# Kernel tuning notes

Measured on AMD Instinct MI355X. Metric: run time of the kernel, lower is better.

## Reference

```python
import jax, jax.numpy as jnp
import numpy as np

B, LAT, H, O, T = 512, 128, 1024, 1, 256


def setup_inputs() -> dict:
    key = jax.random.key(0)
    ks = jax.random.split(key, 8)

    def p(k, shape, fan_in):
        return (jax.random.normal(k, shape, dtype=jnp.float32) / np.sqrt(fan_in)).astype(jnp.float32)

    return {
        "z": jax.random.normal(ks[0], (B, LAT), dtype=jnp.float32),
        # fc_z_to_h / fc_z_to_c
        "Wzh": p(ks[1], (H, LAT), LAT), "bzh": jnp.zeros((H,), jnp.float32),
        "Wzc": p(ks[2], (H, LAT), LAT), "bzc": jnp.zeros((H,), jnp.float32),
        # LSTM (single layer), PyTorch gate order i,f,g,o stacked along dim 0
        "W_ih": p(ks[3], (4 * H, O), max(O, 1)),
        "W_hh": p(ks[4], (4 * H, H), H),
        "b_ih": jnp.zeros((4 * H,), jnp.float32),
        "b_hh": jnp.zeros((4 * H,), jnp.float32),
        # fc_out
        "W_out": p(ks[5], (O, H), H), "b_out": jnp.zeros((O,), jnp.float32),
        "tgt_len": T,
    }


def reference(z, Wzh, bzh, Wzc, bzc, W_ih, W_hh, b_ih, b_hh, W_out, b_out, tgt_len):
    # initial states from latent code
    h = jnp.tanh(z @ Wzh.T + bzh)            # (B, H)
    c = jnp.tanh(z @ Wzc.T + bzc)            # (B, H)
    x0 = jnp.zeros((z.shape[0], W_ih.shape[1]), z.dtype)  # (B, O) zeros start token
    b = b_ih + b_hh

    def step(carry, _):
        h, c, x = carry
        gates = x @ W_ih.T + h @ W_hh.T + b  # (B, 4H)
        i, f, g, o = jnp.split(gates, 4, axis=-1)
        i = jax.nn.sigmoid(i)
        f = jax.nn.sigmoid(f)
        g = jnp.tanh(g)
        o = jax.nn.sigmoid(o)
        c_new = f * c + i * g
        h_new = o * jnp.tanh(c_new)
        y = h_new @ W_out.T + b_out
        return (h_new, c_new, y), y

    _, ys = jax.lax.scan(step, (h, c, x0), None, length=tgt_len)  # (T, B, O)
    return jnp.transpose(ys, (1, 0, 2))      # (B, T, O)
```

## Files before the change

### kernel.cpp

```cpp
#include <hip/hip_runtime.h>

typedef unsigned short u16;
typedef unsigned int u32;
typedef __bf16 bf16x8 __attribute__((ext_vector_type(8)));
typedef float f32x4 __attribute__((ext_vector_type(4)));
typedef u16 u16x8 __attribute__((ext_vector_type(8)));

#define AS1 __attribute__((address_space(1)))
#define AS3 __attribute__((address_space(3)))

constexpr int Bsz = 512;
constexpr int LATn = 128;
constexpr int Hn  = 1024;
constexpr int G4H = 4096;
constexpr int NBLK = 256;

__device__ __forceinline__ u16 f2bf(float x){
  u32 u = __float_as_uint(x);
  return (u16)((u + 0x7FFFu + ((u >> 16) & 1u)) >> 16);
}
__device__ __forceinline__ float bf2f(u16 h){ return __uint_as_float(((u32)h) << 16); }

__device__ __forceinline__ float sigm(float x){
  float e = __builtin_amdgcn_exp2f(x * -1.44269504088896f);
  return __builtin_amdgcn_rcpf(1.0f + e);
}
__device__ __forceinline__ float tanh_f(float x){
  float e = __builtin_amdgcn_exp2f(x * -2.88539008177793f);
  return __builtin_amdgcn_rcpf(1.0f + e) * 2.0f - 1.0f;
}

__device__ __forceinline__ bf16x8 ld8(const u16* p){
  u16x8 v = *reinterpret_cast<const u16x8*>(p);
  return __builtin_bit_cast(bf16x8, v);
}
__device__ __forceinline__ bf16x8 vld8(const volatile u16* p){
  u16x8 v = *reinterpret_cast<const volatile u16x8*>(p);
  return __builtin_bit_cast(bf16x8, v);
}

__device__ __forceinline__ void load16_lds(const u16* g, u16* l){
  __builtin_amdgcn_global_load_lds((AS1 void*)(u16*)g, (AS3 void*)l, 16, 0, 0);
}

__global__ void repack_kernel(
    const float* __restrict__ Whh, const float* __restrict__ b_ih, const float* __restrict__ b_hh,
    const float* __restrict__ Wih, const float* __restrict__ Wout, const float* __restrict__ bout,
    u16* wp, float* bpack, float* wihpack)
{
  const int idx0 = blockIdx.x * blockDim.x + threadIdx.x;
  const int stride = gridDim.x * blockDim.x;
  const float bo = bout[0];
  for (int i = idx0; i < G4H * Hn; i += stride){
    int row = i >> 10, k = i & 1023;
    int g = row >> 10, jj = row & 1023;
    int drow = (jj >> 4) * 64 + g * 16 + (jj & 15);
    float x = Whh[i] + Wout[k] * Wih[row];
    wp[drow * 1024 + k] = f2bf(x);
  }
  for (int i = idx0; i < G4H; i += stride){
    int g = i >> 10, jj = i & 1023;
    int drow = (jj >> 4) * 64 + g * 16 + (jj & 15);
    bpack[drow] = b_ih[i] + b_hh[i] + bo * Wih[i];
    wihpack[drow] = Wih[i];
  }
}

__global__ __launch_bounds__(256, 1) void init_kernel(
    const float* __restrict__ z,
    const float* __restrict__ Wzh, const float* __restrict__ bzh,
    const float* __restrict__ Wzc, const float* __restrict__ bzc,
    const float* __restrict__ Wout, const float* __restrict__ bout,
    u16* hb_hi, u16* hb_lo, float* cbuf, float* yinit)
{
  __shared__ float zrow[LATn];
  __shared__ float yred[256];
  const int b = blockIdx.x, tid = threadIdx.x;
  if (tid < LATn) zrow[tid] = z[b * LATn + tid];
  __syncthreads();
  float ysum = 0.f;
  #pragma unroll
  for (int jj = 0; jj < 4; ++jj){
    const int j = tid * 4 + jj;
    const float* wh = Wzh + (size_t)j * LATn;
    const float* wc = Wzc + (size_t)j * LATn;
    float sh = bzh[j], sc = bzc[j];
    for (int k = 0; k < LATn; ++k){
      const float zv = zrow[k];
      sh = fmaf(zv, wh[k], sh);
      sc = fmaf(zv, wc[k], sc);
    }
    const float h0 = tanh_f(sh);
    cbuf[(size_t)b * Hn + j] = tanh_f(sc);
    const u16 hi = f2bf(h0);
    hb_hi[(size_t)b * Hn + j] = hi;
    hb_lo[(size_t)b * Hn + j] = f2bf(h0 - bf2f(hi));
    ysum = fmaf(h0, Wout[j], ysum);
  }
  yred[tid] = ysum;
  __syncthreads();
  for (int s = 128; s > 0; s >>= 1){
    if (tid < s) yred[tid] += yred[tid + s];
    __syncthreads();
  }
  if (tid == 0) yinit[b] = yred[0] + bout[0];
}

__global__ __launch_bounds__(512, 1) void lstm_xcd(
    const u16* __restrict__ wp,
    const float* __restrict__ bpack, const float* __restrict__ wihpack,
    const float* __restrict__ Wout, const float* __restrict__ bout,
    const float* __restrict__ yinit,
    u16* __restrict__ hb_hi, u16* __restrict__ hb_lo,
    const float* __restrict__ cbuf, float* __restrict__ ypart,
    float* __restrict__ outp, const int* __restrict__ tlen,
    u32* claim, volatile u32* flags)
{
  __shared__ __align__(16) u16 ldsB[4][16384];
  __shared__ int sh_ids[2];

  const int tid = threadIdx.x;
  const int lane = tid & 63, w = tid >> 6;
  const int r = lane & 15, q = lane >> 4;
  const int rowg = w >> 1, jt = w & 1;
  const int T = tlen[0];

  if (tid == 0){
    const int xcd_ = (int)(__builtin_amdgcn_s_getreg(6164) & 7);
    const int slot_ = (int)atomicAdd(&claim[xcd_ * 16], 1u);
    sh_ids[0] = xcd_; sh_ids[1] = slot_;
  }
  __syncthreads();
  const int xcd = sh_ids[0];
  const int slot = sh_ids[1] & 31;

  const int jcol0 = slot * 128;
  const int j = slot * 32 + jt * 16 + r;
  const int row0x = xcd * 64;
  const int wrow0 = row0x + rowg * 16;

  volatile u32* myflag = flags + (size_t)(xcd * 32 + slot) * 16;
  volatile u32* gflag  = flags + (size_t)(xcd * 32) * 16;

  float bias_r[4], wih_r[4];
  #pragma unroll
  for (int nt = 0; nt < 4; ++nt){
    bias_r[nt] = bpack[jcol0 + jt * 64 + nt * 16 + r];
    wih_r[nt]  = wihpack[jcol0 + jt * 64 + nt * 16 + r];
  }
  const float wout_r = Wout[j];
  const float bo = bout[0];

  float creg[4];
  #pragma unroll
  for (int e = 0; e < 4; ++e)
    creg[e] = cbuf[(size_t)(wrow0 + q * 4 + e) * Hn + j];

  const u16* wph = wp + (size_t)jcol0 * 1024;

  auto stage = [&](int c){
    const int buf = c & 3;
    #pragma unroll
    for (int i = 0; i < 4; ++i){
      const int idx = i * 512 + tid;
      const int col = idx >> 4, sp = idx & 15;
      const int sgk = (sp ^ (col & 7)) * 8;
      const int dst = (i * 512 + w * 64) * 8;
      load16_lds(wph + (size_t)col * 1024 + c * 128 + sgk, &ldsB[buf][dst]);
    }
  };

  stage(0); stage(1); stage(2);

  #pragma unroll 1
  for (int t = 0; t < T; ++t){
    const int pb = t & 1;
    const u16* hs_hi = hb_hi + pb * (Bsz * Hn);
    const u16* hs_lo = hb_lo + pb * (Bsz * Hn);
    u16* hd_hi = hb_hi + (pb ^ 1) * (Bsz * Hn);
    u16* hd_lo = hb_lo + (pb ^ 1) * (Bsz * Hn);

    f32x4 acc[4];
    #pragma unroll
    for (int nt = 0; nt < 4; ++nt)
      #pragma unroll
      for (int e = 0; e < 4; ++e)
        acc[nt][e] = bias_r[nt];
    if (t == 0){
      #pragma unroll
      for (int e = 0; e < 4; ++e){
        const float yi = yinit[wrow0 + q * 4 + e];
        #pragma unroll
        for (int nt = 0; nt < 4; ++nt)
          acc[nt][e] -= yi * wih_r[nt];
      }
    }

    const volatile u16* ha_hi = hs_hi + (size_t)(wrow0 + r) * Hn + q * 8;
    const volatile u16* ha_lo = hs_lo + (size_t)(wrow0 + r) * Hn + q * 8;

    #pragma unroll
    for (int c = 0; c < 8; ++c){
      if (c == 0)      asm volatile("s_waitcnt vmcnt(8)"  ::: "memory");
      else if (c == 1) asm volatile("s_waitcnt vmcnt(16)" ::: "memory");
      else if (c == 2) asm volatile("s_waitcnt vmcnt(24)" ::: "memory");
      else if (c <= 5) asm volatile("s_waitcnt vmcnt(32)" ::: "memory");
      else if (c == 6) asm volatile("s_waitcnt vmcnt(28)" ::: "memory");
      else             asm volatile("s_waitcnt vmcnt(24)" ::: "memory");
      __builtin_amdgcn_s_barrier();
      asm volatile("" ::: "memory");

      if (c < 5) stage(c + 3);

      const int buf = c & 3;
      #pragma unroll
      for (int kc = 0; kc < 4; ++kc){
        const int ko = c * 128 + kc * 32;
        const bf16x8 ah = vld8(ha_hi + ko);
        const bf16x8 al = vld8(ha_lo + ko);
        #pragma unroll
        for (int nt = 0; nt < 4; ++nt){
          const int cc = jt * 64 + nt * 16 + r;
          const int phys = (kc * 4 + q) ^ (cc & 7);
          const bf16x8 bh = ld8(&ldsB[buf][(cc * 16 + phys) * 8]);
          acc[nt] = __builtin_amdgcn_mfma_f32_16x16x32_bf16(ah, bh, acc[nt], 0, 0, 0);
          acc[nt] = __builtin_amdgcn_mfma_f32_16x16x32_bf16(al, bh, acc[nt], 0, 0, 0);
        }
      }
    }

    float pp[4];
    #pragma unroll
    for (int e = 0; e < 4; ++e){
      const float gi = sigm(acc[0][e]);
      const float gf = sigm(acc[1][e]);
      const float gg = tanh_f(acc[2][e]);
      const float go = sigm(acc[3][e]);
      const float cn = gf * creg[e] + gi * gg;
      creg[e] = cn;
      const float hn = go * tanh_f(cn);
      const int row = wrow0 + q * 4 + e;
      const u16 hi = f2bf(hn);
      hd_hi[(size_t)row * Hn + j] = hi;
      hd_lo[(size_t)row * Hn + j] = f2bf(hn - bf2f(hi));
      pp[e] = hn * wout_r;
    }
    #pragma unroll
    for (int m = 1; m < 16; m <<= 1)
      #pragma unroll
      for (int e = 0; e < 4; ++e)
        pp[e] += __shfl_xor(pp[e], m, 64);
    if (r == 0){
      #pragma unroll
      for (int e = 0; e < 4; ++e){
        const int row_l = rowg * 16 + q * 4 + e;
        ypart[((size_t)(pb * 8 + xcd) * 64 + row_l) * 64 + slot * 2 + jt] = pp[e];
      }
    }

    __syncthreads();
    if (tid == 0) *myflag = (u32)(t + 1);
    if (t < T - 1){ stage(0); stage(1); stage(2); }

    if (w == 0){
      const u32 tgt = (u32)(t + 1);
      for (int spin = 0; spin < (1 << 17); ++spin){
        const u32 f = (lane < 32) ? gflag[(size_t)lane * 16] : tgt;
        if (__all(f >= tgt)) break;
        __builtin_amdgcn_s_sleep(1);
      }
    }
    __syncthreads();

    if (tid < 64){
      const int rsel = lane >> 5, ll = lane & 31;
      const int row_l = slot * 2 + rsel;
      const volatile float* yp = ypart + ((size_t)(pb * 8 + xcd) * 64 + row_l) * 64;
      float v = yp[ll] + yp[ll + 32];
      #pragma unroll
      for (int m = 1; m < 32; m <<= 1) v += __shfl_xor(v, m, 64);
      if (ll == 0) outp[(size_t)(row0x + row_l) * T + t] = v + bo;
    }
  }
}

extern "C" void kernel_launch(void* const* d_in, const int* in_sizes, int n_in,
                              void* d_out, int out_size, void* d_ws, size_t ws_size,
                              hipStream_t stream)
{
  const float* z    = (const float*)d_in[0];
  const float* Wzh  = (const float*)d_in[1];
  const float* bzh  = (const float*)d_in[2];
  const float* Wzc  = (const float*)d_in[3];
  const float* bzc  = (const float*)d_in[4];
  const float* Wih  = (const float*)d_in[5];
  const float* Whh  = (const float*)d_in[6];
  const float* b_ih = (const float*)d_in[7];
  const float* b_hh = (const float*)d_in[8];
  const float* Wout = (const float*)d_in[9];
  const float* bout = (const float*)d_in[10];
  const int*   tlen = (const int*)d_in[11];
  float* outp = (float*)d_out;

  char* ws = (char*)d_ws;
  size_t off = 0;
  auto alloc = [&](size_t bytes) -> char* {
    char* p = ws + off;
    off += (bytes + 255) & ~size_t(255);
    return p;
  };
  u16* wp     = (u16*)alloc((size_t)G4H * Hn * 2);
  u16* hb_hi  = (u16*)alloc((size_t)2 * Bsz * Hn * 2);
  u16* hb_lo  = (u16*)alloc((size_t)2 * Bsz * Hn * 2);
  float* cbuf    = (float*)alloc((size_t)Bsz * Hn * 4);
  float* yinit   = (float*)alloc((size_t)Bsz * 4);
  float* bpack   = (float*)alloc((size_t)G4H * 4);
  float* wihpack = (float*)alloc((size_t)G4H * 4);
  float* ypart   = (float*)alloc((size_t)2 * 8 * 64 * 64 * 4);
  u32* claim     = (u32*)alloc(8 * 16 * 4);
  u32* flags     = (u32*)alloc((size_t)8 * 32 * 16 * 4);

  (void)hipMemsetAsync(claim, 0, 8 * 16 * 4, stream);
  (void)hipMemsetAsync(flags, 0, (size_t)8 * 32 * 16 * 4, stream);

  repack_kernel<<<dim3(1024), dim3(256), 0, stream>>>(
      Whh, b_ih, b_hh, Wih, Wout, bout, wp, bpack, wihpack);

  init_kernel<<<dim3(Bsz), dim3(256), 0, stream>>>(
      z, Wzh, bzh, Wzc, bzc, Wout, bout, hb_hi, hb_lo, cbuf, yinit);

  lstm_xcd<<<dim3(NBLK), dim3(512), 0, stream>>>(
      wp, bpack, wihpack, Wout, bout, yinit,
      hb_hi, hb_lo, cbuf, ypart, outp, tlen, claim, flags);
}
```

Baseline: 6.860 ms.

## Prefetch h fragments three chunks ahead and split LDS weight tiles by k-half

```diff
diff --git a/kernel.cpp b/kernel.cpp
--- a/kernel.cpp
+++ b/kernel.cpp
@@ -116,7 +116,7 @@
     float* __restrict__ outp, const int* __restrict__ tlen,
     u32* claim, volatile u32* flags)
 {
-  __shared__ __align__(16) u16 ldsB[4][16384];
+  __shared__ __align__(16) u16 ldsB[4][2][8192];
   __shared__ int sh_ids[2];
 
   const int tid = threadIdx.x;
@@ -160,13 +160,15 @@
 
   auto stage = [&](int c){
     const int buf = c & 3;
+    u16* base = (u16*)ldsB[buf];
     #pragma unroll
     for (int i = 0; i < 4; ++i){
-      const int idx = i * 512 + tid;
-      const int col = idx >> 4, sp = idx & 15;
-      const int sgk = (sp ^ (col & 7)) * 8;
-      const int dst = (i * 512 + w * 64) * 8;
-      load16_lds(wph + (size_t)col * 1024 + c * 128 + sgk, &ldsB[buf][dst]);
+      const int S = i * 512 + tid;
+      const int khalf = S >> 10, rem = S & 1023;
+      const int ccw = rem >> 3, sw = rem & 7;
+      const int kk3 = sw ^ (ccw & 7);
+      load16_lds(wph + (size_t)ccw * 1024 + c * 128 + khalf * 64 + kk3 * 8,
+                 base + (i * 512 + w * 64) * 8);
     }
   };
 
@@ -199,14 +201,27 @@
     const volatile u16* ha_hi = hs_hi + (size_t)(wrow0 + r) * Hn + q * 8;
     const volatile u16* ha_lo = hs_lo + (size_t)(wrow0 + r) * Hn + q * 8;
 
+    bf16x8 hh[4][4], hl[4][4];
+    #define HLOAD(cc) {                                        \
+      const int s_ = (cc) & 3;                                 \
+      hh[s_][0] = vld8(ha_hi + (cc) * 128 + 0);                \
+      hl[s_][0] = vld8(ha_lo + (cc) * 128 + 0);                \
+      hh[s_][1] = vld8(ha_hi + (cc) * 128 + 32);               \
+      hl[s_][1] = vld8(ha_lo + (cc) * 128 + 32);               \
+      hh[s_][2] = vld8(ha_hi + (cc) * 128 + 64);               \
+      hl[s_][2] = vld8(ha_lo + (cc) * 128 + 64);               \
+      hh[s_][3] = vld8(ha_hi + (cc) * 128 + 96);               \
+      hl[s_][3] = vld8(ha_lo + (cc) * 128 + 96);               }
+
+    HLOAD(0); HLOAD(1); HLOAD(2);
+
     #pragma unroll
     for (int c = 0; c < 8; ++c){
-      if (c == 0)      asm volatile("s_waitcnt vmcnt(8)"  ::: "memory");
-      else if (c == 1) asm volatile("s_waitcnt vmcnt(16)" ::: "memory");
-      else if (c == 2) asm volatile("s_waitcnt vmcnt(24)" ::: "memory");
-      else if (c <= 5) asm volatile("s_waitcnt vmcnt(32)" ::: "memory");
-      else if (c == 6) asm volatile("s_waitcnt vmcnt(28)" ::: "memory");
-      else             asm volatile("s_waitcnt vmcnt(24)" ::: "memory");
+      if (c == 0)      asm volatile("s_waitcnt vmcnt(16)" ::: "memory");
+      else if (c == 1) asm volatile("s_waitcnt vmcnt(20)" ::: "memory");
+      else if (c <= 5) asm volatile("s_waitcnt vmcnt(24)" ::: "memory");
+      else if (c == 6) asm volatile("s_waitcnt vmcnt(12)" ::: "memory");
+      else             asm volatile("s_waitcnt vmcnt(0)"  ::: "memory");
       __builtin_amdgcn_s_barrier();
       asm volatile("" ::: "memory");
 
@@ -215,19 +230,23 @@
       const int buf = c & 3;
       #pragma unroll
       for (int kc = 0; kc < 4; ++kc){
-        const int ko = c * 128 + kc * 32;
-        const bf16x8 ah = vld8(ha_hi + ko);
-        const bf16x8 al = vld8(ha_lo + ko);
+        const int khalf = kc >> 1;
+        const int kk3 = (kc & 1) * 4 + q;
+        const int s = kk3 ^ (r & 7);
+        const bf16x8 ah = hh[buf][kc];
+        const bf16x8 al = hl[buf][kc];
         #pragma unroll
         for (int nt = 0; nt < 4; ++nt){
           const int cc = jt * 64 + nt * 16 + r;
-          const int phys = (kc * 4 + q) ^ (cc & 7);
-          const bf16x8 bh = ld8(&ldsB[buf][(cc * 16 + phys) * 8]);
+          const bf16x8 bh = ld8(&ldsB[buf][khalf][cc * 64 + s * 8]);
           acc[nt] = __builtin_amdgcn_mfma_f32_16x16x32_bf16(ah, bh, acc[nt], 0, 0, 0);
           acc[nt] = __builtin_amdgcn_mfma_f32_16x16x32_bf16(al, bh, acc[nt], 0, 0, 0);
         }
       }
-    }
+
+      if (c < 5) HLOAD(c + 3);
+    }
+    #undef HLOAD
 
     float pp[4];
     #pragma unroll
```

New measurement: 7.310 ms. 1.07x slower.
